# Optimization experiments

Hardware: AMD Instinct MI355X
Metric: run time of the kernel (lower is better)

The kernel has to match this reference:

```python
import jax, jax.numpy as jnp
import numpy as np
import math

D_MODEL, D_INNER, D_STATE, D_CONV, DT_RANK = 768, 1536, 16, 4, 48
BATCH, SEQLEN = 2, 1024
DT_MIN, DT_MAX = 1e-4, 1.0


def setup_inputs() -> dict:
    key = jax.random.key(0)
    ks = jax.random.split(key, 10)
    D, N, R, K = D_INNER, D_STATE, DT_RANK, D_CONV
    total_out = 2 * D + R + 2 * D * N

    def xavier(k, shape):
        fan_in, fan_out = shape[1], shape[0]
        a = math.sqrt(6.0 / (fan_in + fan_out))
        return jax.random.uniform(k, shape, jnp.float32, -a, a)

    x = jax.random.normal(ks[0], (BATCH, SEQLEN, D_MODEL), jnp.float32)
    W_in = xavier(ks[1], (total_out, D_MODEL))
    W_dt = xavier(ks[2], (D, R))
    W_out = xavier(ks[3], (D_MODEL, D))
    W_res = xavier(ks[4], (D, D_MODEL))
    conv_w = jax.random.normal(ks[5], (D, K), jnp.float32) * (1.0 / math.sqrt(K))
    conv_b = jnp.zeros((D,), jnp.float32)
    # A_log init: log(1..N) per inner channel
    A_log = jnp.broadcast_to(jnp.log(jnp.arange(1, N + 1, dtype=jnp.float32)), (D, N))
    Dskip = jnp.ones((D,), jnp.float32)
    # dt_bias = inverse_softplus(exp(uniform in [log dt_min, log dt_max]))
    dt = jnp.exp(jax.random.uniform(ks[6], (D,), jnp.float32) * (math.log(DT_MAX) - math.log(DT_MIN)) + math.log(DT_MIN))
    dt_bias = dt + jnp.log(-jnp.expm1(-dt))
    norm_w = jnp.ones((D,), jnp.float32)
    ln_w = jnp.ones((D_MODEL,), jnp.float32)
    ln_b = jnp.zeros((D_MODEL,), jnp.float32)
    return {
        "x": x, "ln_w": ln_w, "ln_b": ln_b, "W_in": W_in, "W_dt": W_dt,
        "conv_w": conv_w, "conv_b": conv_b, "A_log": A_log, "Dskip": Dskip,
        "dt_bias": dt_bias, "norm_w": norm_w, "W_res": W_res, "W_out": W_out,
    }


def _forward(x, ln_w, ln_b, W_in, W_dt, conv_w, conv_b, A_log, Dskip, dt_bias, norm_w, W_res, W_out):
    B, L, _ = x.shape
    D, N = A_log.shape
    K = conv_w.shape[1]
    R = W_dt.shape[1]
    # pre LayerNorm
    mu = x.mean(-1, keepdims=True)
    var = ((x - mu) ** 2).mean(-1, keepdims=True)
    xn = (x - mu) * jax.lax.rsqrt(var + 1e-5) * ln_w + ln_b
    # fused input projection, then split
    p = jnp.einsum('bld,od->blo', xn, W_in)  # (B,L,2D+R+2DN)
    z = p[..., :D]
    u = p[..., D:2 * D]
    dth = p[..., 2 * D:2 * D + R]
    Bpar = p[..., 2 * D + R:2 * D + R + D * N].reshape(B, L, D, N)
    Cpar = p[..., 2 * D + R + D * N:].reshape(B, L, D, N)
    # causal depthwise conv over time on u
    uc = jax.lax.conv_general_dilated(
        u.transpose(0, 2, 1), conv_w[:, None, :], (1,), [(K - 1, 0)],
        feature_group_count=D, dimension_numbers=('NCH', 'OIH', 'NCH'))
    u = (uc + conv_b[None, :, None]).transpose(0, 2, 1)  # (B,L,D)
    # dt: low-rank proj + bias -> softplus -> clamp
    dt = jnp.clip(jax.nn.softplus(jnp.einsum('blr,dr->bld', dth, W_dt) + dt_bias), DT_MIN, DT_MAX)
    A = -jnp.exp(A_log)  # (D,N), negative
    dA = jnp.exp(dt[..., None] * A)          # (B,L,D,N)
    dBu = (dt * u)[..., None] * Bpar         # (B,L,D,N)

    def step(h, inp):
        dA_t, dBu_t, C_t = inp               # each (B,D,N)
        h = dA_t * h + dBu_t
        return h, (C_t * h).sum(-1)          # y_t: (B,D)

    h0 = jnp.zeros((B, D, N), x.dtype)
    _, ys = jax.lax.scan(step, h0, (dA.transpose(1, 0, 2, 3),
                                    dBu.transpose(1, 0, 2, 3),
                                    Cpar.transpose(1, 0, 2, 3)))
    y = ys.transpose(1, 0, 2) + u * Dskip    # (B,L,D)
    # fused gated RMSNorm + inner residual
    res = jnp.einsum('blm,dm->bld', x, W_res)
    g = y * jax.nn.silu(z)
    g = g * jax.lax.rsqrt((g * g).mean(-1, keepdims=True) + 1e-6) * norm_w + res
    return jnp.einsum('bld,md->blm', g, W_out)


def reference(x, ln_w, ln_b, W_in, W_dt, conv_w, conv_b, A_log, Dskip, dt_bias, norm_w, W_res, W_out):
    return _forward(x, ln_w, ln_b, W_in, W_dt, conv_w, conv_b, A_log, Dskip, dt_bias, norm_w, W_res, W_out)
```

## Files before the change

kernel.cpp:

```cpp
#include <hip/hip_runtime.h>


typedef unsigned short u16;
typedef __bf16 bf16x8 __attribute__((ext_vector_type(8)));
typedef float f32x4 __attribute__((ext_vector_type(4)));

#define OPAD 52352
#define OTOT 52272
#define DI   1536
#define DM   768
#define Z0   0
#define U0   1536
#define DTH0 3072
#define B0   3120
#define C0   27696

#define SCAN_P 32
#define SCAN_T 32
#define SPF    4

__device__ static inline u16 f2bf(float f) {
    unsigned u = __float_as_uint(f);
    u += 0x7fffu + ((u >> 16) & 1u);
    return (u16)(u >> 16);
}
__device__ static inline float bf2f(u16 s) {
    return __uint_as_float(((unsigned)s) << 16);
}

__device__ static inline void gload16(const void* g, void* l) {
    __builtin_amdgcn_global_load_lds(
        (const __attribute__((address_space(1))) unsigned int*)g,
        (__attribute__((address_space(3))) unsigned int*)l, 16, 0, 0);
}

__device__ static inline void unpack8(uint4 v, float* f) {
    unsigned w0 = v.x, w1 = v.y, w2 = v.z, w3 = v.w;
    f[0] = __uint_as_float(w0 << 16); f[1] = __uint_as_float(w0 & 0xffff0000u);
    f[2] = __uint_as_float(w1 << 16); f[3] = __uint_as_float(w1 & 0xffff0000u);
    f[4] = __uint_as_float(w2 << 16); f[5] = __uint_as_float(w2 & 0xffff0000u);
    f[6] = __uint_as_float(w3 << 16); f[7] = __uint_as_float(w3 & 0xffff0000u);
}

__global__ void cvt_kernel(const float* __restrict__ src, u16* __restrict__ dst,
                           long n_src, long n_tot) {
    long i4 = ((long)blockIdx.x * 256 + threadIdx.x) * 4;
    if (i4 >= n_tot) return;
    ushort4 o;
    if (i4 < n_src) {
        float4 v = *(const float4*)(src + i4);
        o.x = f2bf(v.x); o.y = f2bf(v.y); o.z = f2bf(v.z); o.w = f2bf(v.w);
    } else {
        o.x = o.y = o.z = o.w = 0;
    }
    *(ushort4*)(dst + i4) = o;
}

__device__ static inline void block_reduce2(float& a, float& b) {
    #pragma unroll
    for (int o = 32; o > 0; o >>= 1) {
        a += __shfl_down(a, o);
        b += __shfl_down(b, o);
    }
    __shared__ float sa[4], sb[4];
    int lane = threadIdx.x & 63, w = threadIdx.x >> 6;
    if (lane == 0) { sa[w] = a; sb[w] = b; }
    __syncthreads();
    a = sa[0] + sa[1] + sa[2] + sa[3];
    b = sb[0] + sb[1] + sb[2] + sb[3];
}

__global__ void __launch_bounds__(256) ln_kernel(const float* __restrict__ x,
        const float* __restrict__ w, const float* __restrict__ b,
        u16* __restrict__ xnbf, u16* __restrict__ xbf) {
    int m = blockIdx.x, tid = threadIdx.x;
    const float* xr = x + (size_t)m * DM;
    float v[3];
    v[0] = xr[tid]; v[1] = xr[tid + 256]; v[2] = xr[tid + 512];
    float s = v[0] + v[1] + v[2];
    float ss = v[0]*v[0] + v[1]*v[1] + v[2]*v[2];
    block_reduce2(s, ss);
    float mu = s * (1.f / DM);
    float var = ss * (1.f / DM) - mu * mu;
    float inv = rsqrtf(var + 1e-5f);
    #pragma unroll
    for (int i = 0; i < 3; ++i) {
        int d = tid + i * 256;
        float xn = (v[i] - mu) * inv * w[d] + b[d];
        xnbf[(size_t)m * DM + d] = f2bf(xn);
        xbf[(size_t)m * DM + d] = f2bf(v[i]);
    }
}

template <int OUT_BF16>
__global__ void __launch_bounds__(256) gemm_bt(const u16* __restrict__ A,
        const u16* __restrict__ B, void* __restrict__ C, int K, int ldc) {
    __shared__ u16 smem[2 * 128 * 64];
    u16* As = smem;
    u16* Bs = smem + 128 * 64;
    int tid = threadIdx.x;
    int m0 = blockIdx.x * 128, n0 = blockIdx.y * 128;
    int lane = tid & 63, wave = tid >> 6;
    int wm = wave >> 1, wn = wave & 1;
    int l15 = lane & 15, l4 = lane >> 4;
    f32x4 acc[4][4] = {};
    const u16* Ag = A + (size_t)m0 * K;
    const u16* Bg = B + (size_t)n0 * K;
    int crow = tid >> 3;
    int ccol = ((tid & 7) ^ ((tid >> 3) & 7)) * 8;
    int ldsoff = (tid & 192) * 16;
    int xr = l15 & 7;

    for (int k0 = 0; k0 < K; k0 += 64) {
        __syncthreads();
        #pragma unroll
        for (int it = 0; it < 4; ++it) {
            gload16(Ag + (size_t)(it * 32 + crow) * K + k0 + ccol,
                    (char*)As + it * 4096 + ldsoff);
            gload16(Bg + (size_t)(it * 32 + crow) * K + k0 + ccol,
                    (char*)Bs + it * 4096 + ldsoff);
        }
        __syncthreads();
        const u16* Arow = As + (wm * 64 + l15) * 64;
        const u16* Brow = Bs + (wn * 64 + l15) * 64;
        #pragma unroll
        for (int kk8 = 0; kk8 < 8; kk8 += 4) {
            int sw = ((l4 + kk8) ^ xr) * 8;
            bf16x8 af[4], bfr[4];
            #pragma unroll
            for (int i = 0; i < 4; ++i) af[i] = *(const bf16x8*)(Arow + i * 16 * 64 + sw);
            #pragma unroll
            for (int j = 0; j < 4; ++j) bfr[j] = *(const bf16x8*)(Brow + j * 16 * 64 + sw);
            #pragma unroll
            for (int i = 0; i < 4; ++i)
                #pragma unroll
                for (int j = 0; j < 4; ++j)
                    acc[i][j] = __builtin_amdgcn_mfma_f32_16x16x32_bf16(
                        af[i], bfr[j], acc[i][j], 0, 0, 0);
        }
    }
    #pragma unroll
    for (int i = 0; i < 4; ++i) {
        int row = m0 + wm * 64 + i * 16 + l4 * 4;
        #pragma unroll
        for (int j = 0; j < 4; ++j) {
            int col = n0 + wn * 64 + j * 16 + l15;
            #pragma unroll
            for (int r = 0; r < 4; ++r) {
                size_t off = (size_t)(row + r) * ldc + col;
                if (OUT_BF16) ((u16*)C)[off] = f2bf(acc[i][j][r]);
                else          ((float*)C)[off] = acc[i][j][r];
            }
        }
    }
}

__global__ void __launch_bounds__(256) conv_kernel(const u16* __restrict__ p,
        const float* __restrict__ cw, const float* __restrict__ cb,
        float* __restrict__ u) {
    int d = blockIdx.x * 256 + threadIdx.x;
    int m = blockIdx.y;
    int l = m & 1023;
    int bm = m - l;
    float acc = cb[d];
    #pragma unroll
    for (int j = 0; j < 4; ++j) {
        int ls = l - 3 + j;
        if (ls >= 0)
            acc += cw[d * 4 + j] * bf2f(p[(size_t)(bm + ls) * OPAD + U0 + d]);
    }
    u[(size_t)m * DI + d] = acc;
}

__global__ void __launch_bounds__(256) dt_kernel(const u16* __restrict__ p,
        const float* __restrict__ Wdt, const float* __restrict__ dt_bias,
        float* __restrict__ dt) {
    int m0 = blockIdx.x * 16, tid = threadIdx.x;
    __shared__ float dth_s[16 * 48];
    for (int i = tid; i < 16 * 48; i += 256)
        dth_s[i] = bf2f(p[(size_t)(m0 + i / 48) * OPAD + DTH0 + (i % 48)]);
    __syncthreads();
    #pragma unroll
    for (int ii = 0; ii < 6; ++ii) {
        int d = ii * 256 + tid;
        float base = dt_bias[d];
        float acc[16];
        #pragma unroll
        for (int mm = 0; mm < 16; ++mm) acc[mm] = base;
        for (int r = 0; r < 48; ++r) {
            float wv = Wdt[d * 48 + r];
            #pragma unroll
            for (int mm = 0; mm < 16; ++mm)
                acc[mm] = fmaf(wv, dth_s[mm * 48 + r], acc[mm]);
        }
        #pragma unroll
        for (int mm = 0; mm < 16; ++mm) {
            float xv = acc[mm];
            float sp = xv > 20.f ? xv : log1pf(__expf(xv));
            sp = fminf(fmaxf(sp, 1e-4f), 1.0f);
            dt[(size_t)(m0 + mm) * DI + d] = sp;
        }
    }
}

__global__ void __launch_bounds__(256, 2) scan1_kernel(const u16* __restrict__ p,
        const float* __restrict__ dt, const float* __restrict__ u,
        const float* __restrict__ A_log,
        float* __restrict__ chkA, float* __restrict__ chkB) {
    int d = blockIdx.x * 256 + threadIdx.x;
    int b = blockIdx.y, c = blockIdx.z;
    int t0base = c * SCAN_T;
    float a[16];
    #pragma unroll
    for (int n = 0; n < 16; ++n) a[n] = -__expf(A_log[d * 16 + n]);
    const u16* pB = p + (size_t)(b * 1024 + t0base) * OPAD + B0 + d * 16;
    const float* dtp = dt + (size_t)(b * 1024 + t0base) * DI + d;
    const float* up  = u  + (size_t)(b * 1024 + t0base) * DI + d;
    uint4 Br[SPF][2]; float dtr[SPF], ur[SPF];
    #pragma unroll
    for (int i = 0; i < SPF; ++i) {
        Br[i][0] = *(const uint4*)(pB + (size_t)i * OPAD);
        Br[i][1] = *(const uint4*)(pB + (size_t)i * OPAD + 8);
        dtr[i] = dtp[(size_t)i * DI];
        ur[i]  = up[(size_t)i * DI];
    }
    float h[16], Av[16];
    #pragma unroll
    for (int n = 0; n < 16; ++n) { h[n] = 0.f; Av[n] = 1.f; }
    for (int t0 = 0; t0 < SCAN_T; t0 += SPF) {
        #pragma unroll
        for (int s = 0; s < SPF; ++s) {
            int t = t0 + s;
            uint4 b0 = Br[s][0], b1 = Br[s][1];
            float dtv = dtr[s], uv = ur[s];
            int tl = t + SPF < SCAN_T ? t + SPF : SCAN_T - 1;
            Br[s][0] = *(const uint4*)(pB + (size_t)tl * OPAD);
            Br[s][1] = *(const uint4*)(pB + (size_t)tl * OPAD + 8);
            dtr[s] = dtp[(size_t)tl * DI];
            ur[s]  = up[(size_t)tl * DI];
            float Bf[16];
            unpack8(b0, Bf); unpack8(b1, Bf + 8);
            float dtu = dtv * uv;
            #pragma unroll
            for (int n = 0; n < 16; ++n) {
                float dA = __expf(dtv * a[n]);
                h[n] = fmaf(dA, h[n], dtu * Bf[n]);
                Av[n] *= dA;
            }
        }
    }
    size_t o = (((size_t)c * 2 + b) * 1536 + d) * 16;
    #pragma unroll
    for (int k = 0; k < 4; ++k) {
        *(float4*)(chkA + o + k * 4) = make_float4(Av[4*k], Av[4*k+1], Av[4*k+2], Av[4*k+3]);
        *(float4*)(chkB + o + k * 4) = make_float4(h[4*k], h[4*k+1], h[4*k+2], h[4*k+3]);
    }
}

__global__ void __launch_bounds__(256) scan_comb_kernel(const float* __restrict__ chkA,
        const float* __restrict__ chkB, float* __restrict__ hstart) {
    int idx = blockIdx.x * 256 + threadIdx.x;
    float hs[16];
    #pragma unroll
    for (int n = 0; n < 16; ++n) hs[n] = 0.f;
    for (int c = 0; c < SCAN_P; ++c) {
        size_t o = ((size_t)c * 3072 + idx) * 16;
        #pragma unroll
        for (int k = 0; k < 4; ++k)
            *(float4*)(hstart + o + k * 4) = make_float4(hs[4*k], hs[4*k+1], hs[4*k+2], hs[4*k+3]);
        #pragma unroll
        for (int k = 0; k < 4; ++k) {
            float4 Ac = *(const float4*)(chkA + o + k * 4);
            float4 Bc = *(const float4*)(chkB + o + k * 4);
            hs[4*k]   = fmaf(Ac.x, hs[4*k],   Bc.x);
            hs[4*k+1] = fmaf(Ac.y, hs[4*k+1], Bc.y);
            hs[4*k+2] = fmaf(Ac.z, hs[4*k+2], Bc.z);
            hs[4*k+3] = fmaf(Ac.w, hs[4*k+3], Bc.w);
        }
    }
}

__global__ void __launch_bounds__(256, 2) scan2_kernel(const u16* __restrict__ p,
        const float* __restrict__ dt, const float* __restrict__ u,
        const float* __restrict__ A_log, const float* __restrict__ Dskip,
        const float* __restrict__ hstart, float* __restrict__ y) {
    int d = blockIdx.x * 256 + threadIdx.x;
    int b = blockIdx.y, c = blockIdx.z;
    int t0base = c * SCAN_T;
    float a[16];
    #pragma unroll
    for (int n = 0; n < 16; ++n) a[n] = -__expf(A_log[d * 16 + n]);
    float Dsk = Dskip[d];
    const u16* pB = p + (size_t)(b * 1024 + t0base) * OPAD + B0 + d * 16;
    const u16* pC = p + (size_t)(b * 1024 + t0base) * OPAD + C0 + d * 16;
    const float* dtp = dt + (size_t)(b * 1024 + t0base) * DI + d;
    const float* up  = u  + (size_t)(b * 1024 + t0base) * DI + d;
    float* yp        = y  + (size_t)(b * 1024 + t0base) * DI + d;
    uint4 Br[SPF][2], Cr[SPF][2]; float dtr[SPF], ur[SPF];
    #pragma unroll
    for (int i = 0; i < SPF; ++i) {
        Br[i][0] = *(const uint4*)(pB + (size_t)i * OPAD);
        Br[i][1] = *(const uint4*)(pB + (size_t)i * OPAD + 8);
        Cr[i][0] = *(const uint4*)(pC + (size_t)i * OPAD);
        Cr[i][1] = *(const uint4*)(pC + (size_t)i * OPAD + 8);
        dtr[i] = dtp[(size_t)i * DI];
        ur[i]  = up[(size_t)i * DI];
    }
    float h[16];
    {
        size_t o = ((size_t)c * 3072 + (size_t)b * 1536 + d) * 16;
        #pragma unroll
        for (int k = 0; k < 4; ++k) {
            float4 hv = *(const float4*)(hstart + o + k * 4);
            h[4*k] = hv.x; h[4*k+1] = hv.y; h[4*k+2] = hv.z; h[4*k+3] = hv.w;
        }
    }
    for (int t0 = 0; t0 < SCAN_T; t0 += SPF) {
        #pragma unroll
        for (int s = 0; s < SPF; ++s) {
            int t = t0 + s;
            uint4 b0 = Br[s][0], b1 = Br[s][1], c0 = Cr[s][0], c1 = Cr[s][1];
            float dtv = dtr[s], uv = ur[s];
            int tl = t + SPF < SCAN_T ? t + SPF : SCAN_T - 1;
            Br[s][0] = *(const uint4*)(pB + (size_t)tl * OPAD);
            Br[s][1] = *(const uint4*)(pB + (size_t)tl * OPAD + 8);
            Cr[s][0] = *(const uint4*)(pC + (size_t)tl * OPAD);
            Cr[s][1] = *(const uint4*)(pC + (size_t)tl * OPAD + 8);
            dtr[s] = dtp[(size_t)tl * DI];
            ur[s]  = up[(size_t)tl * DI];
            float Bf[16], Cf[16];
            unpack8(b0, Bf); unpack8(b1, Bf + 8);
            unpack8(c0, Cf); unpack8(c1, Cf + 8);
            float dtu = dtv * uv;
            #pragma unroll
            for (int n = 0; n < 16; ++n) {
                float dA = __expf(dtv * a[n]);
                h[n] = fmaf(dA, h[n], dtu * Bf[n]);
            }
            float a0 = fmaf(Cf[0], h[0], uv * Dsk), a1 = Cf[1] * h[1];
            float a2 = Cf[2] * h[2], a3 = Cf[3] * h[3];
            #pragma unroll
            for (int n = 4; n < 16; n += 4) {
                a0 = fmaf(Cf[n],   h[n],   a0);
                a1 = fmaf(Cf[n+1], h[n+1], a1);
                a2 = fmaf(Cf[n+2], h[n+2], a2);
                a3 = fmaf(Cf[n+3], h[n+3], a3);
            }
            yp[(size_t)t * DI] = (a0 + a1) + (a2 + a3);
        }
    }
}

__global__ void __launch_bounds__(256) gate_kernel(const u16* __restrict__ p,
        const float* __restrict__ y, const float* __restrict__ res,
        const float* __restrict__ norm_w, u16* __restrict__ g) {
    int m = blockIdx.x, tid = threadIdx.x;
    const u16* pz = p + (size_t)m * OPAD + Z0;
    const float* yr = y + (size_t)m * DI;
    float gp[6];
    float ss = 0.f, dummy = 0.f;
    #pragma unroll
    for (int i = 0; i < 6; ++i) {
        int d = i * 256 + tid;
        float z = bf2f(pz[d]);
        float gv = yr[d] * z / (1.f + __expf(-z));
        gp[i] = gv;
        ss += gv * gv;
    }
    block_reduce2(ss, dummy);
    float scale = rsqrtf(ss * (1.f / DI) + 1e-6f);
    #pragma unroll
    for (int i = 0; i < 6; ++i) {
        int d = i * 256 + tid;
        float val = gp[i] * scale * norm_w[d] + res[(size_t)m * DI + d];
        g[(size_t)m * DI + d] = f2bf(val);
    }
}

extern "C" void kernel_launch(void* const* d_in, const int* in_sizes, int n_in,
                              void* d_out, int out_size, void* d_ws, size_t ws_size,
                              hipStream_t stream) {
    const float* x       = (const float*)d_in[0];
    const float* ln_w    = (const float*)d_in[1];
    const float* ln_b    = (const float*)d_in[2];
    const float* W_in    = (const float*)d_in[3];
    const float* W_dt    = (const float*)d_in[4];
    const float* conv_w  = (const float*)d_in[5];
    const float* conv_b  = (const float*)d_in[6];
    const float* A_log   = (const float*)d_in[7];
    const float* Dskip   = (const float*)d_in[8];
    const float* dt_bias = (const float*)d_in[9];
    const float* norm_w  = (const float*)d_in[10];
    const float* W_res   = (const float*)d_in[11];
    const float* W_out   = (const float*)d_in[12];
    float* out = (float*)d_out;

    char* wsb = (char*)d_ws;
    u16* Wbf     = (u16*)(wsb + 0);
    u16* Wresbf  = (u16*)(wsb + 80412672);
    u16* Woutbf  = (u16*)(wsb + 82771968);
    u16* xnbf    = (u16*)(wsb + 85131264);
    u16* xbf     = (u16*)(wsb + 88276992);
    u16* pbuf    = (u16*)(wsb + 91422720);
    float* ucv   = (float*)(wsb + 305856512);
    float* dtv   = (float*)(wsb + 318439424);
    float* ybuf  = (float*)(wsb + 331022336);
    float* resb  = (float*)(wsb + 343605248);
    u16* gbuf    = (u16*)(wsb + 356188160);
    float* chkA  = (float*)(wsb + 0);
    float* chkB  = (float*)(wsb + 6291456);
    float* hst   = (float*)(wsb + 12582912);

    cvt_kernel<<<39264, 256, 0, stream>>>(W_in, Wbf, (long)OTOT * DM, (long)OPAD * DM);
    cvt_kernel<<<1152, 256, 0, stream>>>(W_res, Wresbf, (long)DI * DM, (long)DI * DM);
    cvt_kernel<<<1152, 256, 0, stream>>>(W_out, Woutbf, (long)DM * DI, (long)DM * DI);
    ln_kernel<<<2048, 256, 0, stream>>>(x, ln_w, ln_b, xnbf, xbf);
    gemm_bt<1><<<dim3(16, 409), 256, 0, stream>>>(xnbf, Wbf, pbuf, DM, OPAD);
    gemm_bt<0><<<dim3(16, 12), 256, 0, stream>>>(xbf, Wresbf, resb, DM, DI);
    conv_kernel<<<dim3(6, 2048), 256, 0, stream>>>(pbuf, conv_w, conv_b, ucv);
    dt_kernel<<<128, 256, 0, stream>>>(pbuf, W_dt, dt_bias, dtv);
    scan1_kernel<<<dim3(6, 2, SCAN_P), 256, 0, stream>>>(pbuf, dtv, ucv, A_log, chkA, chkB);
    scan_comb_kernel<<<12, 256, 0, stream>>>(chkA, chkB, hst);
    scan2_kernel<<<dim3(6, 2, SCAN_P), 256, 0, stream>>>(pbuf, dtv, ucv, A_log, Dskip, hst, ybuf);
    gate_kernel<<<2048, 256, 0, stream>>>(pbuf, ybuf, resb, norm_w, gbuf);
    gemm_bt<0><<<dim3(16, 6), 256, 0, stream>>>(gbuf, Woutbf, out, DI, DM);
}
```

Before: 753.7 us.

## Use 256x256 pipelined MFMA GEMM for input projection and widen scan combine

Adds a new 512-thread GEMM kernel with 256x256 output tiles, swizzled double-buffered LDS, interleaved global loads and MFMA phases with priority hints, and uses it for the large input projection. The output padding grows to a multiple of 256 and workspace offsets shift to match. The scan-combine kernel is also rewritten so each thread handles a single state element, launching 192 blocks instead of 12 to raise parallelism. The bigger tile aims to improve operand reuse and hide load latency, at the cost of more LDS and registers per block and some wasted padded columns.

```diff
diff --git a/kernel.cpp b/kernel.cpp
--- a/kernel.cpp
+++ b/kernel.cpp
@@ -5,7 +5,7 @@
 typedef __bf16 bf16x8 __attribute__((ext_vector_type(8)));
 typedef float f32x4 __attribute__((ext_vector_type(4)));
 
-#define OPAD 52352
+#define OPAD 52480
 #define OTOT 52272
 #define DI   1536
 #define DM   768
@@ -155,6 +155,99 @@
     }
 }
 
+#define G2_BUF  65536
+#define G2_HALF 16384
+#define G2_BOFF 32768
+
+__global__ void __launch_bounds__(512, 2) gemm256_bt(const u16* __restrict__ A,
+        const u16* __restrict__ B, u16* __restrict__ C, int K, int ldc) {
+    __shared__ u16 smem[65536];
+    char* smemc = (char*)smem;
+    const int tid = threadIdx.x;
+    const int l = tid & 63, w = tid >> 6;
+    const int wm = w >> 2, wn = w & 3;
+    const int l15 = l & 15, l4 = l >> 4;
+    const int m0 = blockIdx.x * 256, n0 = blockIdx.y * 256;
+    const int NT = K >> 6;
+
+    const int rdoff = l15 * 64 + ((l4 ^ (l15 & 3) ^ ((l15 >> 2) & 3)) << 4);
+    const int segsw = (l & 3) ^ ((l >> 2) & 3) ^ ((l >> 4) & 3);
+    const int srow = w * 32 + (l >> 2);
+    const u16* Ast = A + (size_t)(m0 + srow) * K + segsw * 8;
+    const u16* Bst = B + (size_t)(n0 + srow) * K + segsw * 8;
+    const int sdst = w * 2048;
+
+    f32x4 acc[8][4] = {};
+
+#define G2_STAGE(MATP, MOFF, nxt, sh, tk)                                      \
+    gload16(MATP + (size_t)(tk) * 64 + (sh) * 32,                              \
+            smemc + (nxt) * G2_BUF + (MOFF) + (sh) * G2_HALF + sdst);          \
+    gload16(MATP + (size_t)16 * K + (size_t)(tk) * 64 + (sh) * 32,             \
+            smemc + (nxt) * G2_BUF + (MOFF) + (sh) * G2_HALF + sdst + 1024);
+
+#define G2_PHASE(cur, nxt, rh, h, SMAT, SMOFF, sh, tk, DO_VM)                  \
+    {                                                                          \
+        const char* Ab = smemc + (cur) * G2_BUF + (h) * G2_HALF                \
+                         + (wm * 128 + (rh) * 64) * 64 + rdoff;                \
+        const char* Bb = smemc + (cur) * G2_BUF + G2_BOFF + (h) * G2_HALF      \
+                         + (wn * 64) * 64 + rdoff;                             \
+        bf16x8 af[4], bv[4];                                                   \
+        _Pragma("unroll")                                                      \
+        for (int i = 0; i < 4; ++i) af[i] = *(const bf16x8*)(Ab + i * 1024);   \
+        _Pragma("unroll")                                                      \
+        for (int j = 0; j < 4; ++j) bv[j] = *(const bf16x8*)(Bb + j * 1024);   \
+        G2_STAGE(SMAT, SMOFF, nxt, sh, tk);                                    \
+        __builtin_amdgcn_s_barrier();                                          \
+        __builtin_amdgcn_sched_barrier(0);                                     \
+        __builtin_amdgcn_s_setprio(1);                                         \
+        _Pragma("unroll")                                                      \
+        for (int i = 0; i < 4; ++i)                                            \
+            _Pragma("unroll")                                                  \
+            for (int j = 0; j < 4; ++j)                                        \
+                acc[(rh) * 4 + i][j] = __builtin_amdgcn_mfma_f32_16x16x32_bf16(\
+                    af[i], bv[j], acc[(rh) * 4 + i][j], 0, 0, 0);              \
+        __builtin_amdgcn_s_setprio(0);                                         \
+        __builtin_amdgcn_sched_barrier(0);                                     \
+        if (DO_VM) asm volatile("s_waitcnt vmcnt(4)" ::: "memory");            \
+        __builtin_amdgcn_s_barrier();                                          \
+    }
+
+#define G2_TILE(cur, nxt, tk)                                                  \
+    G2_PHASE(cur, nxt, 0, 0, Ast, 0,       0, tk, 0)                           \
+    G2_PHASE(cur, nxt, 1, 0, Bst, G2_BOFF, 0, tk, 1)                           \
+    G2_PHASE(cur, nxt, 0, 1, Ast, 0,       1, tk, 0)                           \
+    G2_PHASE(cur, nxt, 1, 1, Bst, G2_BOFF, 1, tk, 1)
+
+    G2_STAGE(Ast, 0,       0, 0, 0);
+    G2_STAGE(Bst, G2_BOFF, 0, 0, 0);
+    G2_STAGE(Ast, 0,       0, 1, 0);
+    G2_STAGE(Bst, G2_BOFF, 0, 1, 0);
+    asm volatile("s_waitcnt vmcnt(4)" ::: "memory");
+    __builtin_amdgcn_s_barrier();
+
+    for (int t = 0; t < NT; t += 2) {
+        int tk1 = t + 1;
+        int tk2 = (t + 2 < NT) ? t + 2 : NT - 1;
+        G2_TILE(0, 1, tk1)
+        G2_TILE(1, 0, tk2)
+    }
+
+    #pragma unroll
+    for (int ai = 0; ai < 8; ++ai) {
+        int row = m0 + wm * 128 + ai * 16 + l4 * 4;
+        #pragma unroll
+        for (int j = 0; j < 4; ++j) {
+            int col = n0 + wn * 64 + j * 16 + l15;
+            #pragma unroll
+            for (int r = 0; r < 4; ++r)
+                C[(size_t)(row + r) * ldc + col] = f2bf(acc[ai][j][r]);
+        }
+    }
+#undef G2_STAGE
+#undef G2_PHASE
+#undef G2_TILE
+}
+
 __global__ void __launch_bounds__(256) conv_kernel(const u16* __restrict__ p,
         const float* __restrict__ cw, const float* __restrict__ cb,
         float* __restrict__ u) {
@@ -260,23 +353,11 @@
 __global__ void __launch_bounds__(256) scan_comb_kernel(const float* __restrict__ chkA,
         const float* __restrict__ chkB, float* __restrict__ hstart) {
     int idx = blockIdx.x * 256 + threadIdx.x;
-    float hs[16];
-    #pragma unroll
-    for (int n = 0; n < 16; ++n) hs[n] = 0.f;
+    float hs = 0.f;
     for (int c = 0; c < SCAN_P; ++c) {
-        size_t o = ((size_t)c * 3072 + idx) * 16;
-        #pragma unroll
-        for (int k = 0; k < 4; ++k)
-            *(float4*)(hstart + o + k * 4) = make_float4(hs[4*k], hs[4*k+1], hs[4*k+2], hs[4*k+3]);
-        #pragma unroll
-        for (int k = 0; k < 4; ++k) {
-            float4 Ac = *(const float4*)(chkA + o + k * 4);
-            float4 Bc = *(const float4*)(chkB + o + k * 4);
-            hs[4*k]   = fmaf(Ac.x, hs[4*k],   Bc.x);
-            hs[4*k+1] = fmaf(Ac.y, hs[4*k+1], Bc.y);
-            hs[4*k+2] = fmaf(Ac.z, hs[4*k+2], Bc.z);
-            hs[4*k+3] = fmaf(Ac.w, hs[4*k+3], Bc.w);
-        }
+        size_t o = (size_t)c * 49152 + idx;
+        hstart[o] = hs;
+        hs = fmaf(chkA[o], hs, chkB[o]);
     }
 }
 
@@ -397,30 +478,30 @@
 
     char* wsb = (char*)d_ws;
     u16* Wbf     = (u16*)(wsb + 0);
-    u16* Wresbf  = (u16*)(wsb + 80412672);
-    u16* Woutbf  = (u16*)(wsb + 82771968);
-    u16* xnbf    = (u16*)(wsb + 85131264);
-    u16* xbf     = (u16*)(wsb + 88276992);
-    u16* pbuf    = (u16*)(wsb + 91422720);
-    float* ucv   = (float*)(wsb + 305856512);
-    float* dtv   = (float*)(wsb + 318439424);
-    float* ybuf  = (float*)(wsb + 331022336);
-    float* resb  = (float*)(wsb + 343605248);
-    u16* gbuf    = (u16*)(wsb + 356188160);
+    u16* Wresbf  = (u16*)(wsb + 80609280);
+    u16* Woutbf  = (u16*)(wsb + 82968576);
+    u16* xnbf    = (u16*)(wsb + 85327872);
+    u16* xbf     = (u16*)(wsb + 88473600);
+    u16* pbuf    = (u16*)(wsb + 91619328);
+    float* ucv   = (float*)(wsb + 306577408);
+    float* dtv   = (float*)(wsb + 319160320);
+    float* ybuf  = (float*)(wsb + 331743232);
+    float* resb  = (float*)(wsb + 344326144);
+    u16* gbuf    = (u16*)(wsb + 356909056);
     float* chkA  = (float*)(wsb + 0);
     float* chkB  = (float*)(wsb + 6291456);
     float* hst   = (float*)(wsb + 12582912);
 
-    cvt_kernel<<<39264, 256, 0, stream>>>(W_in, Wbf, (long)OTOT * DM, (long)OPAD * DM);
+    cvt_kernel<<<39360, 256, 0, stream>>>(W_in, Wbf, (long)OTOT * DM, (long)OPAD * DM);
     cvt_kernel<<<1152, 256, 0, stream>>>(W_res, Wresbf, (long)DI * DM, (long)DI * DM);
     cvt_kernel<<<1152, 256, 0, stream>>>(W_out, Woutbf, (long)DM * DI, (long)DM * DI);
     ln_kernel<<<2048, 256, 0, stream>>>(x, ln_w, ln_b, xnbf, xbf);
-    gemm_bt<1><<<dim3(16, 409), 256, 0, stream>>>(xnbf, Wbf, pbuf, DM, OPAD);
+    gemm256_bt<<<dim3(8, 205), 512, 0, stream>>>(xnbf, Wbf, pbuf, DM, OPAD);
     gemm_bt<0><<<dim3(16, 12), 256, 0, stream>>>(xbf, Wresbf, resb, DM, DI);
     conv_kernel<<<dim3(6, 2048), 256, 0, stream>>>(pbuf, conv_w, conv_b, ucv);
     dt_kernel<<<128, 256, 0, stream>>>(pbuf, W_dt, dt_bias, dtv);
     scan1_kernel<<<dim3(6, 2, SCAN_P), 256, 0, stream>>>(pbuf, dtv, ucv, A_log, chkA, chkB);
-    scan_comb_kernel<<<12, 256, 0, stream>>>(chkA, chkB, hst);
+    scan_comb_kernel<<<192, 256, 0, stream>>>(chkA, chkB, hst);
     scan2_kernel<<<dim3(6, 2, SCAN_P), 256, 0, stream>>>(pbuf, dtv, ucv, A_log, Dskip, hst, ybuf);
     gate_kernel<<<2048, 256, 0, stream>>>(pbuf, ybuf, resb, norm_w, gbuf);
     gemm_bt<0><<<dim3(16, 6), 256, 0, stream>>>(gbuf, Woutbf, out, DI, DM);
```

After: 728.6 us. 1.03x faster.
